# Optimization experiments

Hardware: AMD Instinct MI355X
Metric: run time of the kernel (lower is better)

Reference implementation:

```python
import jax, jax.numpy as jnp
import numpy as np

N_ROIS = 512
N_EDGES = N_ROIS * N_ROIS
N_VIEWS = 6
DIMS = [(1, 36), (36, 24), (24, 5)]  # (in, out) for conv1..3


def _init_params(key):
    params = []
    for li, (cin, cout) in enumerate(DIMS):
        k = jax.random.fold_in(key, li)
        k1, k2, k3 = jax.random.split(k, 3)
        lw = jax.random.normal(k1, (N_VIEWS, cin * cout), dtype=jnp.float32) * 0.1
        lb = jnp.zeros((cin * cout,), dtype=jnp.float32)
        root = jax.random.normal(k2, (cin, cout), dtype=jnp.float32) * 0.1
        b = jnp.zeros((cout,), dtype=jnp.float32)
        params += [lw, lb, root, b]
    return params


def setup_inputs() -> dict:
    key = jax.random.key(0)
    k1, k2, k3 = jax.random.split(key, 3)
    x = jnp.ones((N_ROIS, 1), dtype=jnp.float32)
    edge_attr = jax.random.uniform(k1, (N_EDGES, N_VIEWS), dtype=jnp.float32)
    edge_index = jax.random.randint(k2, (2, N_EDGES), 0, N_ROIS, dtype=jnp.int64)
    p = _init_params(k3)
    names = []
    for i in (1, 2, 3):
        names += [f"lw{i}", f"lb{i}", f"root{i}", f"b{i}"]
    out = {"x": x, "edge_attr": edge_attr, "edge_index": edge_index}
    out.update(dict(zip(names, p)))
    return out


def _nnconv(x, edge_index, edge_attr, lw, lb, root, b, cin, cout):
    # Edge MLP: Linear + ReLU -> per-edge weight matrix [E, cin, cout]
    w = jax.nn.relu(edge_attr @ lw + lb).reshape(-1, cin, cout)
    src, dst = edge_index[0], edge_index[1]
    # gather source node features, per-edge matmul
    msg = jnp.einsum('ei,eio->eo', x[src], w)  # [E, cout]
    ssum = jax.ops.segment_sum(msg, dst, num_segments=N_ROIS)
    cnt = jax.ops.segment_sum(jnp.ones((msg.shape[0],), dtype=x.dtype), dst,
                              num_segments=N_ROIS)
    aggr = ssum / jnp.maximum(cnt, 1.0)[:, None]  # mean aggregation
    return aggr + x @ root + b  # root weight + bias (PyG NNConv defaults)


def reference(x, edge_attr, edge_index,
              lw1, lb1, root1, b1,
              lw2, lb2, root2, b2,
              lw3, lb3, root3, b3):
    h = jax.nn.relu(_nnconv(x, edge_index, edge_attr, lw1, lb1, root1, b1, *DIMS[0]))
    h = jax.nn.relu(_nnconv(h, edge_index, edge_attr, lw2, lb2, root2, b2, *DIMS[1]))
    h = jax.nn.relu(_nnconv(h, edge_index, edge_attr, lw3, lb3, root3, b3, *DIMS[2]))
    # cbt[i, j] = sum_k |h[i,k] - h[j,k]|  (repeat/transpose/abs/sum tail)
    cbt = jnp.sum(jnp.abs(h[:, None, :] - h[None, :, :]), axis=2)  # [N, N]
    return cbt
```

## Files before the change

kernel.cpp:

```cpp
#include <hip/hip_runtime.h>

#define NROIS 512
#define NEDGES 262144

__device__ __forceinline__ int detect_i64(const unsigned* __restrict__ er) {
    unsigned acc = 0;
#pragma unroll
    for (int i = 0; i < 64; ++i) acc |= er[2 * i + 1];
    return acc == 0u;
}

__device__ __forceinline__ void load_edge(const unsigned* __restrict__ er,
                                          bool i64, int e, int& src, int& dst) {
    if (i64) { src = (int)er[2 * e]; dst = (int)er[2 * NEDGES + 2 * e]; }
    else     { src = (int)er[e];     dst = (int)er[NEDGES + e]; }
}

__global__ __launch_bounds__(256) void hist_kernel(const unsigned* __restrict__ er,
                                                   int* __restrict__ gpart)
{
    __shared__ int lh[NROIS];
    __shared__ int s_l;
    const int t = threadIdx.x;
    if (t == 0) s_l = detect_i64(er);
    for (int i = t; i < NROIS; i += 256) lh[i] = 0;
    __syncthreads();
    const bool L = (s_l != 0);
    const int e0 = blockIdx.x * 4096;
#pragma unroll
    for (int k = 0; k < 16; ++k) {
        int e = e0 + k * 256 + t, src, dst;
        load_edge(er, L, e, src, dst);
        atomicAdd(&lh[dst], 1);
    }
    __syncthreads();
    for (int i = t; i < NROIS; i += 256) gpart[blockIdx.x * NROIS + i] = lh[i];
}

__global__ __launch_bounds__(512) void scan_kernel(const int* __restrict__ gpart,
                                                   int* __restrict__ start,
                                                   int* __restrict__ cursor)
{
    __shared__ int tmp[NROIS];
    const int t = threadIdx.x;
    int own = 0;
#pragma unroll 8
    for (int b = 0; b < 64; ++b) own += gpart[b * NROIS + t];
    tmp[t] = own;
    __syncthreads();
    for (int off = 1; off < NROIS; off <<= 1) {
        int v = tmp[t];
        int add = (t >= off) ? tmp[t - off] : 0;
        __syncthreads();
        tmp[t] = v + add;
        __syncthreads();
    }
    start[t + 1] = tmp[t];
    if (t == 0) start[0] = 0;
    cursor[t] = tmp[t] - own;
}

__global__ __launch_bounds__(256) void scatter_kernel(const unsigned* __restrict__ er,
                                                      const float* __restrict__ ea,
                                                      int* __restrict__ gcursor,
                                                      unsigned* __restrict__ perm,
                                                      float* __restrict__ eas,
                                                      int packed)
{
    __shared__ int lh[NROIS];
    __shared__ int lbase[NROIS];
    __shared__ int s_l;
    const int t = threadIdx.x;
    if (t == 0) s_l = detect_i64(er);
    for (int i = t; i < NROIS; i += 256) lh[i] = 0;
    __syncthreads();
    const bool L = (s_l != 0);
    const int e0 = blockIdx.x * 1024;
#pragma unroll
    for (int k = 0; k < 4; ++k) {
        int e = e0 + k * 256 + t, src, dst;
        load_edge(er, L, e, src, dst);
        atomicAdd(&lh[dst], 1);
    }
    __syncthreads();
    for (int i = t; i < NROIS; i += 256) {
        int c = lh[i];
        lbase[i] = c ? atomicAdd(&gcursor[i], c) : 0;
    }
    __syncthreads();
#pragma unroll
    for (int k = 0; k < 4; ++k) {
        int e = e0 + k * 256 + t, src, dst;
        load_edge(er, L, e, src, dst);
        int pos = atomicAdd(&lbase[dst], 1);
        unsigned ps = ((unsigned)e << 9) | (unsigned)src;
        if (packed) {
            const float2* s = reinterpret_cast<const float2*>(ea + (size_t)e * 6);
            const float2 a0 = s[0], a1 = s[1], a2 = s[2];
            float4* d = reinterpret_cast<float4*>(eas + (size_t)pos * 8);
            d[0] = make_float4(a0.x, a0.y, a1.x, a1.y);
            d[1] = make_float4(a2.x, a2.y, __uint_as_float(ps), 0.f);
        } else {
            perm[pos] = ps;
        }
    }
}

template <int CIN, int COUT, int STR, bool PACKED>
__global__ __launch_bounds__(256) void layer_kernel(
    const float* __restrict__ eas, const float* __restrict__ ea,
    const unsigned* __restrict__ perm, const int* __restrict__ start,
    const float* __restrict__ lw, const float* __restrict__ lb,
    const float* __restrict__ root, const float* __restrict__ bias,
    const float* __restrict__ hin, float* __restrict__ hout)
{
    __shared__ float sh[NROIS * STR];
    __shared__ float red[4 * COUT];
    const int t = threadIdx.x;

    for (int idx = t; idx < NROIS * CIN; idx += 256) {
        const int r = idx / CIN;
        sh[r * STR + (idx - r * CIN)] = hin[idx];
    }
    __syncthreads();

    const int dst = blockIdx.x;
    const int s0 = start[dst], c1 = start[dst + 1];
    const int cnt = c1 - s0;

    float acc[COUT];
#pragma unroll
    for (int o = 0; o < COUT; ++o) acc[o] = 0.f;

    for (int idx = s0 + t; idx < c1; idx += 256) {
        float a0, a1, a2, a3, a4, a5;
        unsigned ps;
        if constexpr (PACKED) {
            const float4* __restrict__ base = reinterpret_cast<const float4*>(eas);
            const float4 r0 = base[2 * idx], r1 = base[2 * idx + 1];
            a0 = r0.x; a1 = r0.y; a2 = r0.z; a3 = r0.w;
            a4 = r1.x; a5 = r1.y; ps = __float_as_uint(r1.z);
        } else {
            ps = perm[idx];
            const float* __restrict__ ap = ea + (size_t)(ps >> 9) * 6;
            a0 = ap[0]; a1 = ap[1]; a2 = ap[2]; a3 = ap[3]; a4 = ap[4]; a5 = ap[5];
        }
        const int hbase = (int)(ps & 511u) * STR;

#pragma unroll 2
        for (int i = 0; i < CIN; ++i) {
            const float hsv = sh[hbase + i];
#pragma unroll
            for (int o = 0; o < COUT; ++o) {
                float tt = lb[i * COUT + o];
                tt = fmaf(a0, lw[0 * (CIN * COUT) + i * COUT + o], tt);
                tt = fmaf(a1, lw[1 * (CIN * COUT) + i * COUT + o], tt);
                tt = fmaf(a2, lw[2 * (CIN * COUT) + i * COUT + o], tt);
                tt = fmaf(a3, lw[3 * (CIN * COUT) + i * COUT + o], tt);
                tt = fmaf(a4, lw[4 * (CIN * COUT) + i * COUT + o], tt);
                tt = fmaf(a5, lw[5 * (CIN * COUT) + i * COUT + o], tt);
                acc[o] = fmaf(hsv, fmaxf(tt, 0.f), acc[o]);
            }
        }
    }

#pragma unroll
    for (int o = 0; o < COUT; ++o) {
        float v = acc[o];
#pragma unroll
        for (int d = 32; d > 0; d >>= 1) v += __shfl_xor(v, d);
        acc[o] = v;
    }
    const int lane = t & 63, wid = t >> 6;
    if (lane == 0) {
#pragma unroll
        for (int o = 0; o < COUT; ++o) red[wid * COUT + o] = acc[o];
    }
    __syncthreads();

    if (t < COUT) {
        float tot = red[t] + red[COUT + t] + red[2 * COUT + t] + red[3 * COUT + t];
        float aggr = tot / fmaxf((float)cnt, 1.f);
        float r = bias[t];
#pragma unroll 4
        for (int k = 0; k < CIN; ++k)
            r = fmaf(sh[dst * STR + k], root[k * COUT + t], r);
        hout[dst * COUT + t] = fmaxf(aggr + r, 0.f);
    }
}

__global__ __launch_bounds__(256) void cbt_kernel(const float* __restrict__ h,
                                                  float* __restrict__ out)
{
    __shared__ float sh[NROIS * 5];
    for (int t = threadIdx.x; t < NROIS * 5; t += 256) sh[t] = h[t];
    __syncthreads();
    const int i = blockIdx.x;
    float hi[5];
#pragma unroll
    for (int k = 0; k < 5; ++k) hi[k] = sh[i * 5 + k];
    for (int j = threadIdx.x; j < NROIS; j += 256) {
        float s = 0.f;
#pragma unroll
        for (int k = 0; k < 5; ++k) s += fabsf(hi[k] - sh[j * 5 + k]);
        out[i * NROIS + j] = s;
    }
}

template <bool PACKED>
static void run_layers(const float* x, const float* ea,
                       const float* lw1, const float* lb1, const float* root1, const float* b1,
                       const float* lw2, const float* lb2, const float* root2, const float* b2,
                       const float* lw3, const float* lb3, const float* root3, const float* b3,
                       const float* eas, const unsigned* perm, const int* start,
                       float* h1, float* h2, float* h3, hipStream_t stream)
{
    layer_kernel<1, 36, 1, PACKED><<<NROIS, 256, 0, stream>>>(
        eas, ea, perm, start, lw1, lb1, root1, b1, x, h1);
    layer_kernel<36, 24, 37, PACKED><<<NROIS, 256, 0, stream>>>(
        eas, ea, perm, start, lw2, lb2, root2, b2, h1, h2);
    layer_kernel<24, 5, 25, PACKED><<<NROIS, 256, 0, stream>>>(
        eas, ea, perm, start, lw3, lb3, root3, b3, h2, h3);
}

extern "C" void kernel_launch(void* const* d_in, const int* in_sizes, int n_in,
                              void* d_out, int out_size, void* d_ws, size_t ws_size,
                              hipStream_t stream)
{
    const float*    x     = (const float*)d_in[0];
    const float*    ea    = (const float*)d_in[1];
    const unsigned* er    = (const unsigned*)d_in[2];
    const float*    lw1   = (const float*)d_in[3];
    const float*    lb1   = (const float*)d_in[4];
    const float*    root1 = (const float*)d_in[5];
    const float*    b1    = (const float*)d_in[6];
    const float*    lw2   = (const float*)d_in[7];
    const float*    lb2   = (const float*)d_in[8];
    const float*    root2 = (const float*)d_in[9];
    const float*    b2    = (const float*)d_in[10];
    const float*    lw3   = (const float*)d_in[11];
    const float*    lb3   = (const float*)d_in[12];
    const float*    root3 = (const float*)d_in[13];
    const float*    b3    = (const float*)d_in[14];

    const size_t easN  = (size_t)NEDGES * 8;
    const size_t restN = 18432 + 12288 + 2560 + 131072 + 513 + 512 + NEDGES;
    const size_t needPacked = (easN + restN) * 4;
    const int packed = (ws_size >= needPacked) ? 1 : 0;

    float* ws   = (float*)d_ws;
    float* eas  = ws;
    float* rest = packed ? (ws + easN) : ws;
    float* h1   = rest;
    float* h2   = h1 + NROIS * 36;
    float* h3   = h2 + NROIS * 24;
    int* gpart  = (int*)(h3 + NROIS * 5);
    int* start  = gpart + 131072;
    int* cursor = start + NROIS + 1;
    unsigned* perm = (unsigned*)(cursor + NROIS);

    hist_kernel<<<NEDGES / 4096, 256, 0, stream>>>(er, gpart);
    scan_kernel<<<1, 512, 0, stream>>>(gpart, start, cursor);
    scatter_kernel<<<NEDGES / 1024, 256, 0, stream>>>(er, ea, cursor, perm, eas, packed);

    if (packed)
        run_layers<true>(x, ea, lw1, lb1, root1, b1, lw2, lb2, root2, b2,
                         lw3, lb3, root3, b3, eas, perm, start, h1, h2, h3, stream);
    else
        run_layers<false>(x, ea, lw1, lb1, root1, b1, lw2, lb2, root2, b2,
                          lw3, lb3, root3, b3, eas, perm, start, h1, h2, h3, stream);

    cbt_kernel<<<NROIS, 256, 0, stream>>>(h3, (float*)d_out);
}
```

Baseline: 161.5 us.

## Use 512-thread blocks with occupancy hints and uniform predicated edge loop in layer kernels

Layer kernels now launch 512 threads per block with launch-bounds min-waves hints, so each destination node's roughly 512 edges map to about one pass per thread. The edge loop gets a uniform trip count: out-of-range lanes read a clamped edge and point at a zeroed shared-memory row instead of branching. This targets per-block tail imbalance and divergence. The risk is register pressure or spills from the tighter occupancy hints, especially in the 36x24 layer.

```diff
diff --git a/kernel.cpp b/kernel.cpp
--- a/kernel.cpp
+++ b/kernel.cpp
@@ -106,22 +106,24 @@
     }
 }
 
-template <int CIN, int COUT, int STR, bool PACKED>
-__global__ __launch_bounds__(256) void layer_kernel(
+template <int CIN, int COUT, int STR, int BLOCK, int MINW, bool PACKED>
+__global__ __launch_bounds__(BLOCK, MINW) void layer_kernel(
     const float* __restrict__ eas, const float* __restrict__ ea,
     const unsigned* __restrict__ perm, const int* __restrict__ start,
     const float* __restrict__ lw, const float* __restrict__ lb,
     const float* __restrict__ root, const float* __restrict__ bias,
     const float* __restrict__ hin, float* __restrict__ hout)
 {
-    __shared__ float sh[NROIS * STR];
-    __shared__ float red[4 * COUT];
-    const int t = threadIdx.x;
-
-    for (int idx = t; idx < NROIS * CIN; idx += 256) {
+    constexpr int NW = BLOCK / 64;
+    __shared__ float sh[NROIS * STR + CIN];
+    __shared__ float red[NW * COUT];
+    const int t = threadIdx.x;
+
+    for (int idx = t; idx < NROIS * CIN; idx += BLOCK) {
         const int r = idx / CIN;
         sh[r * STR + (idx - r * CIN)] = hin[idx];
     }
+    if (t < CIN) sh[NROIS * STR + t] = 0.f;
     __syncthreads();
 
     const int dst = blockIdx.x;
@@ -132,20 +134,24 @@
 #pragma unroll
     for (int o = 0; o < COUT; ++o) acc[o] = 0.f;
 
-    for (int idx = s0 + t; idx < c1; idx += 256) {
+    const int nr = (cnt + BLOCK - 1) / BLOCK;
+    for (int r = 0; r < nr; ++r) {
+        const int idx = s0 + r * BLOCK + t;
+        const bool val = (idx < c1);
+        const int eidx = val ? idx : s0;
         float a0, a1, a2, a3, a4, a5;
         unsigned ps;
         if constexpr (PACKED) {
             const float4* __restrict__ base = reinterpret_cast<const float4*>(eas);
-            const float4 r0 = base[2 * idx], r1 = base[2 * idx + 1];
+            const float4 r0 = base[2 * eidx], r1 = base[2 * eidx + 1];
             a0 = r0.x; a1 = r0.y; a2 = r0.z; a3 = r0.w;
             a4 = r1.x; a5 = r1.y; ps = __float_as_uint(r1.z);
         } else {
-            ps = perm[idx];
+            ps = perm[eidx];
             const float* __restrict__ ap = ea + (size_t)(ps >> 9) * 6;
             a0 = ap[0]; a1 = ap[1]; a2 = ap[2]; a3 = ap[3]; a4 = ap[4]; a5 = ap[5];
         }
-        const int hbase = (int)(ps & 511u) * STR;
+        const int hbase = val ? (int)(ps & 511u) * STR : NROIS * STR;
 
 #pragma unroll 2
         for (int i = 0; i < CIN; ++i) {
@@ -179,13 +185,15 @@
     __syncthreads();
 
     if (t < COUT) {
-        float tot = red[t] + red[COUT + t] + red[2 * COUT + t] + red[3 * COUT + t];
+        float tot = 0.f;
+#pragma unroll
+        for (int w = 0; w < NW; ++w) tot += red[w * COUT + t];
         float aggr = tot / fmaxf((float)cnt, 1.f);
-        float r = bias[t];
+        float rr = bias[t];
 #pragma unroll 4
         for (int k = 0; k < CIN; ++k)
-            r = fmaf(sh[dst * STR + k], root[k * COUT + t], r);
-        hout[dst * COUT + t] = fmaxf(aggr + r, 0.f);
+            rr = fmaf(sh[dst * STR + k], root[k * COUT + t], rr);
+        hout[dst * COUT + t] = fmaxf(aggr + rr, 0.f);
     }
 }
 
@@ -215,11 +223,11 @@
                        const float* eas, const unsigned* perm, const int* start,
                        float* h1, float* h2, float* h3, hipStream_t stream)
 {
-    layer_kernel<1, 36, 1, PACKED><<<NROIS, 256, 0, stream>>>(
+    layer_kernel<1, 36, 1, 512, 6, PACKED><<<NROIS, 512, 0, stream>>>(
         eas, ea, perm, start, lw1, lb1, root1, b1, x, h1);
-    layer_kernel<36, 24, 37, PACKED><<<NROIS, 256, 0, stream>>>(
+    layer_kernel<36, 24, 37, 512, 4, PACKED><<<NROIS, 512, 0, stream>>>(
         eas, ea, perm, start, lw2, lb2, root2, b2, h1, h2);
-    layer_kernel<24, 5, 25, PACKED><<<NROIS, 256, 0, stream>>>(
+    layer_kernel<24, 5, 25, 512, 6, PACKED><<<NROIS, 512, 0, stream>>>(
         eas, ea, perm, start, lw3, lb3, root3, b3, h2, h3);
 }
 
```

Result: slower. 189.1 us (+17.1%).
